# Kernel optimization log

Hardware: AMD Instinct MI355X
Metric: run time of the kernel (lower is better)

Reference implementation:

```python
import jax, jax.numpy as jnp
import numpy as np

N_NODES = 20000
N_EDGES = 200000
C = 64             # channel multiplicity (hidden_irreps = 64x0e + 64x1o)
LMAX = 3
NLM = (LMAX + 1) ** 2   # 16 spherical-harmonic components
NUM_ELEM = 10
R_DIM = 8          # radial embedding out dim
MLP_H = 64
AVG_NEI = 10.0
L_OF_LM = np.repeat(np.arange(LMAX + 1), 2 * np.arange(LMAX + 1) + 1)  # [16] l index per lm slot


def setup_inputs() -> dict:
    key = jax.random.key(0)
    k = jax.random.split(key, 16)
    f32 = jnp.float32
    elems = jax.random.randint(k[0], (N_NODES,), 0, NUM_ELEM)
    one_hot = jax.nn.one_hot(elems, NUM_ELEM, dtype=f32)
    node_features = jax.random.normal(k[1], (N_NODES, C), dtype=f32)
    angular_embedding = jax.random.normal(k[2], (N_EDGES, NLM), dtype=f32)
    radial_embedding = jax.random.normal(k[3], (N_EDGES, R_DIM), dtype=f32)
    edge_index = jax.random.randint(k[4], (2, N_EDGES), 0, N_NODES)

    def w(kk, shape, fan_in):  # e3nn-style 1/sqrt(fan_in) normalization baked into init
        return jax.random.normal(kk, shape, dtype=f32) / float(np.sqrt(fan_in))

    W_up = w(k[5], (C, C), C)
    W_mlp1 = w(k[6], (R_DIM, MLP_H), R_DIM)
    W_mlp2 = w(k[7], (MLP_H, MLP_H), MLP_H)
    W_mlp3 = w(k[8], (MLP_H, MLP_H), MLP_H)
    W_mlp4 = w(k[9], (MLP_H, (LMAX + 1) * C), MLP_H)
    W_lin = w(k[10], (LMAX + 1, C, C), C)
    W_skip = w(k[11], (C, NUM_ELEM, C), C * NUM_ELEM)
    W_c0 = jax.random.normal(k[12], (NUM_ELEM, C), dtype=f32)
    W_c1 = jax.random.normal(k[13], (NUM_ELEM, C), dtype=f32)
    W_p0 = w(k[14], (C, C), C)
    W_p1 = w(k[15], (C, C), C)
    return dict(node_features=node_features, one_hot=one_hot,
                angular_embedding=angular_embedding, radial_embedding=radial_embedding,
                W_up=W_up, W_mlp1=W_mlp1, W_mlp2=W_mlp2, W_mlp3=W_mlp3, W_mlp4=W_mlp4,
                W_lin=W_lin, W_skip=W_skip, W_c0=W_c0, W_c1=W_c1, W_p0=W_p0, W_p1=W_p1,
                edge_index=edge_index)


def reference(node_features, one_hot, angular_embedding, radial_embedding,
              W_up, W_mlp1, W_mlp2, W_mlp3, W_mlp4, W_lin, W_skip,
              W_c0, W_c1, W_p0, W_p1, edge_index):
    sender, receiver = edge_index[0], edge_index[1]
    n = node_features.shape[0]
    # ---- interaction block (RealAgnosticResidual; node feats are pure scalars 64x0e) ----
    x = node_features @ W_up                                    # linear_up [N,C]
    h = jax.nn.silu(radial_embedding @ W_mlp1)                  # radial MLP -> per-edge TP weights
    h = jax.nn.silu(h @ W_mlp2)
    h = jax.nn.silu(h @ W_mlp3)
    tp_w = (h @ W_mlp4).reshape(-1, LMAX + 1, C)                # [E,4,C] (one weight per l path, uvu)
    w_lm = tp_w[:, L_OF_LM, :]                                  # [E,16,C]
    # uvu tensor product of 0e node feats with spherical harmonics (CG trivial for 0e x l -> l)
    msg = x[sender][:, None, :] * angular_embedding[:, :, None] * w_lm   # [E,16,C]
    agg = jax.ops.segment_sum(msg, receiver, num_segments=n) / AVG_NEI   # scatter-sum [N,16,C]
    feats = jnp.einsum('nmc,mck->nmk', agg, W_lin[L_OF_LM])     # per-l channel-mixing linear [N,16,C]
    # residual skip FCTP(64x0e, 10x0e -> hidden): only the 0e block is connected
    sc0 = jnp.einsum('nc,na,cak->nk', node_features, one_hot, W_skip)    # [N,C]
    # ---- equivariant product basis block (correlation = 1) ----
    wn0 = one_hot @ W_c0                                        # element-dependent weights [N,C]
    wn1 = one_hot @ W_c1
    f0 = feats[:, 0, :] * wn0                                   # l=0 output [N,C]
    f1 = feats[:, 1:4, :] * wn1[:, None, :]                     # l=1 output [N,3,C]
    out0 = f0 @ W_p0 + sc0                                      # [N,C]
    out1 = jnp.einsum('nmc,ck->nmk', f1, W_p1)                  # [N,3,C] (sc 1o block is zero)
    # flatten to e3nn channel-major irreps layout -> node_env [N, C*(1+3)]
    return jnp.concatenate([out0, jnp.swapaxes(out1, 1, 2).reshape(n, -1)], axis=-1)
```

## Files before the change

### kernel.cpp

```cpp
#include <hip/hip_runtime.h>

typedef __attribute__((ext_vector_type(8))) short s16x8;
typedef __attribute__((ext_vector_type(4))) float f32x4;

__device__ inline float bf2f(ushort u) {
    union { unsigned int i; float f; } v; v.i = ((unsigned)u) << 16; return v.f;
}
__device__ inline float u2f(unsigned u) {
    union { unsigned int i; float f; } v; v.i = u; return v.f;
}
__device__ inline ushort f2bf(float f) {
    union { float f; unsigned int i; } v; v.f = f;
    unsigned r = v.i + 0x7FFFu + ((v.i >> 16) & 1u);
    return (ushort)(r >> 16);
}
__device__ inline unsigned cvt_pk(float lo, float hi) {
    unsigned d;
    asm("v_cvt_pk_bf16_f32 %0, %1, %2" : "=v"(d) : "v"(lo), "v"(hi));
    return d;
}
__device__ inline float silu_f(float x) {
    float e;
    asm("v_exp_f32 %0, %1" : "=v"(e) : "v"(x * -1.44269504f));
    float d = 1.f + e, r;
    asm("v_rcp_f32 %0, %1" : "=v"(r) : "v"(d));
    return x * r;
}

__global__ __launch_bounds__(256) void prep_up_kernel(
    const float* __restrict__ nf, const float* __restrict__ W_up,
    ushort* __restrict__ x_ws,
    const float* __restrict__ W1, const float* __restrict__ W2,
    const float* __restrict__ W3, const float* __restrict__ W4,
    const float* __restrict__ W_lin, const float* __restrict__ Wp0,
    const float* __restrict__ Wp1, const float* __restrict__ W_skip,
    ushort* __restrict__ wimg, int* __restrict__ counts, int N) {
    __shared__ float sW[64 * 64];
    __shared__ float sNf[32][64];
    int tid = threadIdx.x;
    int nub = N / 32;
    if ((int)blockIdx.x < nub) {
        size_t n0 = (size_t)blockIdx.x * 32;
        for (int i = tid; i < 4096; i += 256) sW[i] = W_up[i];
        for (int i = tid; i < 2048; i += 256) {
            int r = i >> 6, c = i & 63;
            sNf[r][c] = nf[(n0 + r) * 64 + c];
        }
        __syncthreads();
        int r = tid >> 3, k0 = (tid & 7) * 8;
        float acc[8] = {0, 0, 0, 0, 0, 0, 0, 0};
        #pragma unroll 4
        for (int c = 0; c < 64; ++c) {
            float v = sNf[r][c];
            const float* wr = &sW[c * 64 + k0];
            #pragma unroll
            for (int j = 0; j < 8; ++j) acc[j] += v * wr[j];
        }
        uint4 val;
        val.x = cvt_pk(acc[0], acc[1]);
        val.y = cvt_pk(acc[2], acc[3]);
        val.z = cvt_pk(acc[4], acc[5]);
        val.w = cvt_pk(acc[6], acc[7]);
        *(uint4*)(x_ws + (n0 + r) * 64 + k0) = val;
        return;
    }
    int idx = ((int)blockIdx.x - nub) * 256 + tid;
    if (idx < N) counts[idx] = 0;
    if (idx < 4096) {
        int m = idx >> 6, k = idx & 63;
        int dst = m * 64 + ((((k >> 3) ^ (m & 7))) << 3) + (k & 7);
        wimg[dst] = (k < 8) ? f2bf(W1[k * 64 + m]) : (ushort)0;
    } else if (idx < 8192) {
        int i = idx - 4096;
        int m = i >> 6, k = i & 63;
        int dst = 4096 + m * 64 + ((((k >> 3) ^ (m & 7))) << 3) + (k & 7);
        wimg[dst] = f2bf(W2[k * 64 + m]);
    } else if (idx < 12288) {
        int i = idx - 8192;
        int m = i >> 6, k = i & 63;
        int dst = 8192 + m * 64 + ((((k >> 3) ^ (m & 7))) << 3) + (k & 7);
        wimg[dst] = f2bf(W3[k * 64 + m]);
    } else if (idx < 20480) {
        int i = idx - 12288;
        int m = i >> 6, k = i & 63;
        int dst = 12288 + m * 64 + ((((k >> 3) ^ (m & 7))) << 3) + (k & 7);
        wimg[dst] = f2bf(W4[k * 256 + m]);
    } else if (idx < 29696) {
        int i = idx - 20480;
        int row = i / 72, k = i % 72;
        int l = row >> 6, col = row & 63;
        wimg[idx] = (k < 64) ? f2bf(W_lin[l * 4096 + k * 64 + col]) : (ushort)0;
    } else if (idx < 38912) {
        int i = idx - 29696;
        int row = i / 72, k = i % 72;
        int l = row >> 6, col = row & 63;
        const float* Wp = l ? Wp1 : Wp0;
        wimg[idx] = (k < 64) ? f2bf(Wp[k * 64 + col]) : (ushort)0;
    } else if (idx < 79872) {
        int i = idx - 38912;
        wimg[idx] = f2bf(W_skip[i]);
    }
}

__global__ __launch_bounds__(256) void hist_kernel(const int* __restrict__ recv,
                                                   int* __restrict__ counts, int E) {
    int e = blockIdx.x * 256 + threadIdx.x;
    if (e < E) atomicAdd(&counts[recv[e]], 1);
}

__global__ __launch_bounds__(1024) void scan_kernel(const int* __restrict__ counts,
                                                    int* __restrict__ offsets,
                                                    int* __restrict__ cursor, int n) {
    __shared__ int wsums[16];
    int tid = threadIdx.x, lane = tid & 63, wid = tid >> 6;
    int CH = (n + 1023) >> 10;
    int base = tid * CH;
    int cnt[20];
    int tot = 0;
    if (CH <= 20) {
        #pragma unroll
        for (int j = 0; j < 20; ++j) {
            int i = base + j;
            cnt[j] = (j < CH && i < n) ? counts[i] : 0;
            tot += cnt[j];
        }
    } else {
        for (int j = 0; j < CH; ++j) {
            int i = base + j;
            if (i < n) tot += counts[i];
        }
    }
    int v = tot;
    for (int off = 1; off < 64; off <<= 1) {
        int t = __shfl_up(v, off, 64);
        if (lane >= off) v += t;
    }
    if (lane == 63) wsums[wid] = v;
    __syncthreads();
    if (tid == 0) {
        int acc = 0;
        for (int w = 0; w < 16; ++w) { int t = wsums[w]; wsums[w] = acc; acc += t; }
    }
    __syncthreads();
    int excl = wsums[wid] + v - tot;
    if (CH <= 20) {
        #pragma unroll
        for (int j = 0; j < 20; ++j) {
            int i = base + j;
            if (j < CH && i < n) {
                offsets[i] = excl; cursor[i] = excl; excl += cnt[j];
            }
        }
    } else {
        for (int j = 0; j < CH; ++j) {
            int i = base + j;
            if (i < n) { offsets[i] = excl; cursor[i] = excl; excl += counts[i]; }
        }
    }
    if (tid == 1023) offsets[n] = excl;
}

__global__ __launch_bounds__(256) void scatter_kernel(const int* __restrict__ recv,
                                                      const int* __restrict__ sender,
                                                      const float* __restrict__ angular,
                                                      const float* __restrict__ radial,
                                                      int* __restrict__ cursor,
                                                      int* __restrict__ csr_sender,
                                                      float4* __restrict__ csr_ang,
                                                      ushort* __restrict__ csr_radb, int E) {
    int e = blockIdx.x * 256 + threadIdx.x;
    if (e < E) {
        int r = recv[e];
        int pos = atomicAdd(&cursor[r], 1);
        csr_sender[pos] = sender[e];
        csr_ang[pos] = *(const float4*)(angular + (size_t)e * 16);
        float4 r0 = *(const float4*)(radial + (size_t)e * 8);
        float4 r1 = *(const float4*)(radial + (size_t)e * 8 + 4);
        uint2 lo = {cvt_pk(r0.x, r0.y), cvt_pk(r0.z, r0.w)};
        uint2 hi = {cvt_pk(r1.x, r1.y), cvt_pk(r1.z, r1.w)};
        *(uint2*)(csr_radb + (size_t)pos * 8) = lo;
        *(uint2*)(csr_radb + (size_t)pos * 8 + 4) = hi;
    }
}

__global__ __launch_bounds__(256) void edge_mlp_kernel(const ushort* __restrict__ csr_radb,
                                                       const ushort* __restrict__ wimg,
                                                       unsigned* __restrict__ tpw32, int E) {
    __shared__ __align__(16) ushort sW4[8192];
    __shared__ __align__(16) ushort sB[4][1024];
    int tid = threadIdx.x, lane = tid & 63, wave = tid >> 6;
    int n = lane & 15, hi = lane >> 4;

    for (int i = tid; i < 1024; i += 256)
        ((s16x8*)sW4)[i] = ((const s16x8*)(wimg + 12288))[i];

    s16x8 w1f[4], w2f[4][2], w3f[4][2];
    #pragma unroll
    for (int mt = 0; mt < 4; ++mt) {
        int row = mt * 16 + n, r7 = row & 7;
        w1f[mt] = *(const s16x8*)(wimg + row * 64 + ((hi ^ r7) << 3));
        #pragma unroll
        for (int ks = 0; ks < 2; ++ks) {
            w2f[mt][ks] = *(const s16x8*)(wimg + 4096 + row * 64 + (((ks * 4 + hi) ^ r7) << 3));
            w3f[mt][ks] = *(const s16x8*)(wimg + 8192 + row * 64 + (((ks * 4 + hi) ^ r7) << 3));
        }
    }
    __syncthreads();

    char* myB = (char*)sB[wave];
    int n7 = n & 7;

    for (int sub = 0; sub < 2; ++sub) {
        int base = blockIdx.x * 128 + wave * 32 + sub * 16;
        if (base >= E) break;
        int pos16 = min(base + n, E - 1);

        s16x8 bR;
        #pragma unroll
        for (int j = 0; j < 8; ++j) bR[j] = 0;
        if (hi == 0) bR = *(const s16x8*)(csr_radb + (size_t)pos16 * 8);

        f32x4 zero = {0.f, 0.f, 0.f, 0.f};
        f32x4 d[4];
        #pragma unroll
        for (int mt = 0; mt < 4; ++mt)
            d[mt] = __builtin_amdgcn_mfma_f32_16x16x32_bf16(w1f[mt], bR, zero, 0, 0, 0);

        #pragma unroll
        for (int mt = 0; mt < 4; ++mt) {
            uint2 val = {cvt_pk(silu_f(d[mt][0]), silu_f(d[mt][1])),
                         cvt_pk(silu_f(d[mt][2]), silu_f(d[mt][3]))};
            int slot = mt * 2 + (hi >> 1);
            *(uint2*)(myB + n * 128 + ((slot ^ n7) << 4) + (hi & 1) * 8) = val;
        }
        s16x8 b0 = *(const s16x8*)(myB + n * 128 + ((hi ^ n7) << 4));
        s16x8 b1 = *(const s16x8*)(myB + n * 128 + (((4 + hi) ^ n7) << 4));

        #pragma unroll
        for (int mt = 0; mt < 4; ++mt) {
            d[mt] = __builtin_amdgcn_mfma_f32_16x16x32_bf16(w2f[mt][0], b0, zero, 0, 0, 0);
            d[mt] = __builtin_amdgcn_mfma_f32_16x16x32_bf16(w2f[mt][1], b1, d[mt], 0, 0, 0);
        }
        #pragma unroll
        for (int mt = 0; mt < 4; ++mt) {
            uint2 val = {cvt_pk(silu_f(d[mt][0]), silu_f(d[mt][1])),
                         cvt_pk(silu_f(d[mt][2]), silu_f(d[mt][3]))};
            int slot = mt * 2 + (hi >> 1);
            *(uint2*)(myB + n * 128 + ((slot ^ n7) << 4) + (hi & 1) * 8) = val;
        }
        b0 = *(const s16x8*)(myB + n * 128 + ((hi ^ n7) << 4));
        b1 = *(const s16x8*)(myB + n * 128 + (((4 + hi) ^ n7) << 4));

        #pragma unroll
        for (int mt = 0; mt < 4; ++mt) {
            d[mt] = __builtin_amdgcn_mfma_f32_16x16x32_bf16(w3f[mt][0], b0, zero, 0, 0, 0);
            d[mt] = __builtin_amdgcn_mfma_f32_16x16x32_bf16(w3f[mt][1], b1, d[mt], 0, 0, 0);
        }
        #pragma unroll
        for (int mt = 0; mt < 4; ++mt) {
            uint2 val = {cvt_pk(silu_f(d[mt][0]), silu_f(d[mt][1])),
                         cvt_pk(silu_f(d[mt][2]), silu_f(d[mt][3]))};
            int slot = mt * 2 + (hi >> 1);
            *(uint2*)(myB + n * 128 + ((slot ^ n7) << 4) + (hi & 1) * 8) = val;
        }
        b0 = *(const s16x8*)(myB + n * 128 + ((hi ^ n7) << 4));
        b1 = *(const s16x8*)(myB + n * 128 + (((4 + hi) ^ n7) << 4));

        f32x4 o[8];
        #pragma unroll
        for (int mt = 0; mt < 8; ++mt) {
            int row = mt * 16 + n, r7 = row & 7;
            s16x8 a0f = *(const s16x8*)(sW4 + row * 64 + ((hi ^ r7) << 3));
            s16x8 a1f = *(const s16x8*)(sW4 + row * 64 + (((4 + hi) ^ r7) << 3));
            o[mt] = __builtin_amdgcn_mfma_f32_16x16x32_bf16(a0f, b0, zero, 0, 0, 0);
            o[mt] = __builtin_amdgcn_mfma_f32_16x16x32_bf16(a1f, b1, o[mt], 0, 0, 0);
        }
        if ((base + n) < E) {
            size_t rowbase = (size_t)(base + n) * 64;
            #pragma unroll
            for (int mt = 0; mt < 4; ++mt) {
                uint4 val;
                val.x = cvt_pk(o[mt][0], o[mt + 4][0]);
                val.y = cvt_pk(o[mt][1], o[mt + 4][1]);
                val.z = cvt_pk(o[mt][2], o[mt + 4][2]);
                val.w = cvt_pk(o[mt][3], o[mt + 4][3]);
                *(uint4*)(tpw32 + rowbase + mt * 16 + hi * 4) = val;
            }
        }
    }
}

__global__ __launch_bounds__(256) void agg_kernel(const float4* __restrict__ csr_ang,
                                                  const int* __restrict__ csr_sender,
                                                  const unsigned* __restrict__ tpw32,
                                                  const int* __restrict__ offsets,
                                                  const ushort* __restrict__ x_ws,
                                                  ushort* __restrict__ agg, int N) {
    int wave = threadIdx.x >> 6, lane = threadIdx.x & 63;
    int node = blockIdx.x * 4 + wave;
    if (node >= N) return;
    int beg = offsets[node], end = offsets[node + 1];
    float a0 = 0, a1 = 0, a2 = 0, a3 = 0;
    for (int cb = beg; cb < end; cb += 64) {
        int m = min(64, end - cb);
        int sv = csr_sender[cb + min(lane, m - 1)];
        for (int e0 = 0; e0 < m; e0 += 4) {
            unsigned t[4];
            ushort x[4];
            float4 g[4];
            #pragma unroll
            for (int j = 0; j < 4; ++j) {
                int e = e0 + j;
                int ec = min(e, m - 1);
                t[j] = tpw32[(size_t)(cb + ec) * 64 + lane];
                x[j] = x_ws[(size_t)__shfl(sv, ec) * 64 + lane];
                if (e < m) g[j] = csr_ang[cb + e];
                else g[j] = make_float4(0.f, 0.f, 0.f, 0.f);
            }
            #pragma unroll
            for (int j = 0; j < 4; ++j) {
                float xv = bf2f(x[j]);
                float tp0 = u2f(t[j] << 16);
                float tp1 = u2f(t[j] & 0xffff0000u);
                float y0 = xv * tp0, y1 = xv * tp1;
                a0 += g[j].x * y0;
                a1 += g[j].y * y1;
                a2 += g[j].z * y1;
                a3 += g[j].w * y1;
            }
        }
    }
    size_t b = (size_t)node * 256 + lane;
    agg[b] = f2bf(a0 * 0.1f);
    agg[b + 64] = f2bf(a1 * 0.1f);
    agg[b + 128] = f2bf(a2 * 0.1f);
    agg[b + 192] = f2bf(a3 * 0.1f);
}

__global__ __launch_bounds__(256) void node_out2_kernel(
    const float* __restrict__ nf, const float* __restrict__ one_hot,
    const ushort* __restrict__ wimg, const float* __restrict__ W_c0,
    const float* __restrict__ W_c1, const ushort* __restrict__ agg,
    float* __restrict__ out) {
    __shared__ __align__(16) ushort sWl[2 * 64 * 72];
    __shared__ __align__(16) ushort sF[4][32 * 72];
    __shared__ float sSc[32][64];
    __shared__ float sWc[2][640];
    __shared__ int sElem[32];
    int tid = threadIdx.x;
    int n0 = blockIdx.x * 32;
    int lane = tid & 63, m = tid >> 6;
    int lsel = (m == 0) ? 0 : 1;

    s16x8 pf[4][2];
    #pragma unroll
    for (int nt = 0; nt < 4; ++nt)
        #pragma unroll
        for (int ks = 0; ks < 2; ++ks)
            pf[nt][ks] = *(const s16x8*)(wimg + 29696 +
                (lsel * 64 + nt * 16 + (lane & 15)) * 72 + ks * 32 + (lane >> 4) * 8);

    for (int i = tid; i < 1152; i += 256)
        ((s16x8*)sWl)[i] = ((const s16x8*)(wimg + 20480))[i];
    for (int i = tid; i < 1280; i += 256)
        sWc[i >= 640][i % 640] = (i >= 640 ? W_c1 : W_c0)[i % 640];
    if (tid < 32) {
        int nn = n0 + tid, e = 0;
        for (int a = 0; a < 10; ++a)
            if (one_hot[(size_t)nn * 10 + a] > 0.5f) { e = a; break; }
        sElem[tid] = e;
    }
    __syncthreads();

    {
        int nl = tid >> 3, k0 = (tid & 7) * 8;
        int nn = n0 + nl, elem = sElem[nl];
        float acc[8] = {0, 0, 0, 0, 0, 0, 0, 0};
        const ushort* wskb = wimg + 38912;
        for (int c = 0; c < 64; ++c) {
            float v = nf[(size_t)nn * 64 + c];
            s16x8 w = *(const s16x8*)(wskb + ((size_t)c * 10 + elem) * 64 + k0);
            #pragma unroll
            for (int j = 0; j < 8; ++j) acc[j] += v * bf2f((ushort)w[j]);
        }
        #pragma unroll
        for (int j = 0; j < 8; ++j) sSc[nl][k0 + j] = acc[j];
    }

    f32x4 acc[2][4] = {};
    s16x8 afr[2][2];
    #pragma unroll
    for (int mt = 0; mt < 2; ++mt)
        #pragma unroll
        for (int ks = 0; ks < 2; ++ks)
            afr[mt][ks] = *(const s16x8*)(agg +
                (((size_t)(n0 + mt * 16 + (lane & 15))) * 4 + m) * 64 +
                ks * 32 + (lane >> 4) * 8);
    #pragma unroll
    for (int nt = 0; nt < 4; ++nt)
        #pragma unroll
        for (int ks = 0; ks < 2; ++ks) {
            s16x8 b = *(const s16x8*)(sWl + (lsel * 64 + nt * 16 + (lane & 15)) * 72 +
                                      ks * 32 + (lane >> 4) * 8);
            #pragma unroll
            for (int mt = 0; mt < 2; ++mt)
                acc[mt][nt] = __builtin_amdgcn_mfma_f32_16x16x32_bf16(afr[mt][ks], b,
                                                                      acc[mt][nt], 0, 0, 0);
        }

    #pragma unroll
    for (int mt = 0; mt < 2; ++mt)
        #pragma unroll
        for (int nt = 0; nt < 4; ++nt)
            #pragma unroll
            for (int r = 0; r < 4; ++r) {
                int nl = mt * 16 + (lane >> 4) * 4 + r;
                int k = nt * 16 + (lane & 15);
                float scale = sWc[lsel][sElem[nl] * 64 + k];
                sF[m][nl * 72 + k] = f2bf(acc[mt][nt][r] * scale);
            }
    __syncthreads();

    f32x4 acc2[2][4] = {};
    s16x8 af2[2][2];
    #pragma unroll
    for (int mt = 0; mt < 2; ++mt)
        #pragma unroll
        for (int ks = 0; ks < 2; ++ks)
            af2[mt][ks] = *(const s16x8*)(&sF[m][(mt * 16 + (lane & 15)) * 72 +
                                                 ks * 32 + (lane >> 4) * 8]);
    #pragma unroll
    for (int nt = 0; nt < 4; ++nt)
        #pragma unroll
        for (int ks = 0; ks < 2; ++ks) {
            #pragma unroll
            for (int mt = 0; mt < 2; ++mt)
                acc2[mt][nt] = __builtin_amdgcn_mfma_f32_16x16x32_bf16(af2[mt][ks],
                                                                       pf[nt][ks],
                                                                       acc2[mt][nt], 0, 0, 0);
        }

    #pragma unroll
    for (int mt = 0; mt < 2; ++mt)
        #pragma unroll
        for (int nt = 0; nt < 4; ++nt)
            #pragma unroll
            for (int r = 0; r < 4; ++r) {
                int nl = mt * 16 + (lane >> 4) * 4 + r;
                int k = nt * 16 + (lane & 15);
                size_t nn = (size_t)n0 + nl;
                if (m == 0)
                    out[nn * 256 + k] = acc2[mt][nt][r] + sSc[nl][k];
                else
                    out[nn * 256 + 64 + k * 3 + (m - 1)] = acc2[mt][nt][r];
            }
}

extern "C" void kernel_launch(void* const* d_in, const int* in_sizes, int n_in,
                              void* d_out, int out_size, void* d_ws, size_t ws_size,
                              hipStream_t stream) {
    const float* node_features = (const float*)d_in[0];
    const float* one_hot = (const float*)d_in[1];
    const float* angular = (const float*)d_in[2];
    const float* radial = (const float*)d_in[3];
    const float* W_up = (const float*)d_in[4];
    const float* W_mlp1 = (const float*)d_in[5];
    const float* W_mlp2 = (const float*)d_in[6];
    const float* W_mlp3 = (const float*)d_in[7];
    const float* W_mlp4 = (const float*)d_in[8];
    const float* W_lin = (const float*)d_in[9];
    const float* W_skip = (const float*)d_in[10];
    const float* W_c0 = (const float*)d_in[11];
    const float* W_c1 = (const float*)d_in[12];
    const float* W_p0 = (const float*)d_in[13];
    const float* W_p1 = (const float*)d_in[14];
    const int* edge_index = (const int*)d_in[15];
    float* out = (float*)d_out;

    int N = in_sizes[0] / 64;
    int E = in_sizes[2] / 16;
    const int* sender = edge_index;
    const int* receiver = edge_index + E;

    char* p = (char*)d_ws;
    ushort* x_ws = (ushort*)p;      p += (size_t)N * 64 * 2;
    unsigned* tpw32 = (unsigned*)p; p += (size_t)E * 64 * 4;
    ushort* agg = (ushort*)p;       p += (size_t)N * 256 * 2;
    ushort* wimg = (ushort*)p;      p += 79872 * 2;
    float4* csr_ang = (float4*)p;   p += (size_t)E * 16;
    ushort* csr_radb = (ushort*)p;  p += (size_t)E * 8 * 2;
    int* counts = (int*)p;          p += (size_t)N * 4;
    int* offsets = (int*)p;         p += (size_t)(N + 1) * 4;
    int* cursor = (int*)p;          p += (size_t)N * 4;
    int* csr_sender = (int*)p;      p += (size_t)E * 4;

    prep_up_kernel<<<N / 32 + 312, 256, 0, stream>>>(node_features, W_up, x_ws,
                                                     W_mlp1, W_mlp2, W_mlp3, W_mlp4,
                                                     W_lin, W_p0, W_p1, W_skip, wimg,
                                                     counts, N);
    hist_kernel<<<(E + 255) / 256, 256, 0, stream>>>(receiver, counts, E);
    scan_kernel<<<1, 1024, 0, stream>>>(counts, offsets, cursor, N);
    scatter_kernel<<<(E + 255) / 256, 256, 0, stream>>>(receiver, sender, angular,
                                                        radial, cursor, csr_sender,
                                                        csr_ang, csr_radb, E);
    edge_mlp_kernel<<<(E + 127) / 128, 256, 0, stream>>>(csr_radb, wimg, tpw32, E);
    agg_kernel<<<(N + 3) / 4, 256, 0, stream>>>(csr_ang, csr_sender, tpw32, offsets,
                                                x_ws, agg, N);
    node_out2_kernel<<<N / 32, 256, 0, stream>>>(node_features, one_hot, wimg,
                                                 W_c0, W_c1, agg, out);
}
```

Measured before the change: 129.6 us.

## Fuse CSR scatter into edge MLP kernel, writing tensor-product weights at CSR slots

```diff
diff --git a/kernel.cpp b/kernel.cpp
--- a/kernel.cpp
+++ b/kernel.cpp
@@ -160,32 +160,12 @@
     if (tid == 1023) offsets[n] = excl;
 }
 
-__global__ __launch_bounds__(256) void scatter_kernel(const int* __restrict__ recv,
-                                                      const int* __restrict__ sender,
-                                                      const float* __restrict__ angular,
-                                                      const float* __restrict__ radial,
-                                                      int* __restrict__ cursor,
-                                                      int* __restrict__ csr_sender,
-                                                      float4* __restrict__ csr_ang,
-                                                      ushort* __restrict__ csr_radb, int E) {
-    int e = blockIdx.x * 256 + threadIdx.x;
-    if (e < E) {
-        int r = recv[e];
-        int pos = atomicAdd(&cursor[r], 1);
-        csr_sender[pos] = sender[e];
-        csr_ang[pos] = *(const float4*)(angular + (size_t)e * 16);
-        float4 r0 = *(const float4*)(radial + (size_t)e * 8);
-        float4 r1 = *(const float4*)(radial + (size_t)e * 8 + 4);
-        uint2 lo = {cvt_pk(r0.x, r0.y), cvt_pk(r0.z, r0.w)};
-        uint2 hi = {cvt_pk(r1.x, r1.y), cvt_pk(r1.z, r1.w)};
-        *(uint2*)(csr_radb + (size_t)pos * 8) = lo;
-        *(uint2*)(csr_radb + (size_t)pos * 8 + 4) = hi;
-    }
-}
-
-__global__ __launch_bounds__(256) void edge_mlp_kernel(const ushort* __restrict__ csr_radb,
-                                                       const ushort* __restrict__ wimg,
-                                                       unsigned* __restrict__ tpw32, int E) {
+__global__ __launch_bounds__(256) void edge_mlp_kernel(
+    const int* __restrict__ recv, const int* __restrict__ sender,
+    const float* __restrict__ angular, const float* __restrict__ radial,
+    int* __restrict__ cursor, int* __restrict__ csr_sender,
+    float4* __restrict__ csr_ang, const ushort* __restrict__ wimg,
+    unsigned* __restrict__ tpw32, int E) {
     __shared__ __align__(16) ushort sW4[8192];
     __shared__ __align__(16) ushort sB[4][1024];
     int tid = threadIdx.x, lane = tid & 63, wave = tid >> 6;
@@ -213,12 +193,31 @@
     for (int sub = 0; sub < 2; ++sub) {
         int base = blockIdx.x * 128 + wave * 32 + sub * 16;
         if (base >= E) break;
-        int pos16 = min(base + n, E - 1);
+        int e = base + n;
+        bool oke = e < E;
+        int eC = min(e, E - 1);
 
         s16x8 bR;
         #pragma unroll
         for (int j = 0; j < 8; ++j) bR[j] = 0;
-        if (hi == 0) bR = *(const s16x8*)(csr_radb + (size_t)pos16 * 8);
+        int pos = 0;
+        if (hi == 0) {
+            float4 r0 = *(const float4*)(radial + (size_t)eC * 8);
+            float4 r1 = *(const float4*)(radial + (size_t)eC * 8 + 4);
+            union { s16x8 v; uint4 u; } bb;
+            bb.u.x = cvt_pk(r0.x, r0.y);
+            bb.u.y = cvt_pk(r0.z, r0.w);
+            bb.u.z = cvt_pk(r1.x, r1.y);
+            bb.u.w = cvt_pk(r1.z, r1.w);
+            bR = bb.v;
+            if (oke) {
+                int r = recv[e];
+                pos = atomicAdd(&cursor[r], 1);
+                csr_sender[pos] = sender[e];
+                csr_ang[pos] = *(const float4*)(angular + (size_t)e * 16);
+            }
+        }
+        pos = __shfl(pos, n);
 
         f32x4 zero = {0.f, 0.f, 0.f, 0.f};
         f32x4 d[4];
@@ -275,8 +274,8 @@
             o[mt] = __builtin_amdgcn_mfma_f32_16x16x32_bf16(a0f, b0, zero, 0, 0, 0);
             o[mt] = __builtin_amdgcn_mfma_f32_16x16x32_bf16(a1f, b1, o[mt], 0, 0, 0);
         }
-        if ((base + n) < E) {
-            size_t rowbase = (size_t)(base + n) * 64;
+        if (oke) {
+            size_t rowbase = (size_t)pos * 64;
             #pragma unroll
             for (int mt = 0; mt < 4; ++mt) {
                 uint4 val;
@@ -488,7 +487,6 @@
     ushort* agg = (ushort*)p;       p += (size_t)N * 256 * 2;
     ushort* wimg = (ushort*)p;      p += 79872 * 2;
     float4* csr_ang = (float4*)p;   p += (size_t)E * 16;
-    ushort* csr_radb = (ushort*)p;  p += (size_t)E * 8 * 2;
     int* counts = (int*)p;          p += (size_t)N * 4;
     int* offsets = (int*)p;         p += (size_t)(N + 1) * 4;
     int* cursor = (int*)p;          p += (size_t)N * 4;
@@ -500,10 +498,9 @@
                                                      counts, N);
     hist_kernel<<<(E + 255) / 256, 256, 0, stream>>>(receiver, counts, E);
     scan_kernel<<<1, 1024, 0, stream>>>(counts, offsets, cursor, N);
-    scatter_kernel<<<(E + 255) / 256, 256, 0, stream>>>(receiver, sender, angular,
-                                                        radial, cursor, csr_sender,
-                                                        csr_ang, csr_radb, E);
-    edge_mlp_kernel<<<(E + 127) / 128, 256, 0, stream>>>(csr_radb, wimg, tpw32, E);
+    edge_mlp_kernel<<<(E + 127) / 128, 256, 0, stream>>>(receiver, sender, angular,
+                                                         radial, cursor, csr_sender,
+                                                         csr_ang, wimg, tpw32, E);
     agg_kernel<<<(N + 3) / 4, 256, 0, stream>>>(csr_ang, csr_sender, tpw32, offsets,
                                                 x_ws, agg, N);
     node_out2_kernel<<<N / 32, 256, 0, stream>>>(node_features, one_hot, wimg,
```

Measured after the change: 117.6 us. -9.3%, faster.
